# Performance work log

Hardware: AMD Instinct MI355X
Metric: run time of the kernel (lower is better)

## Reference

```python
import jax, jax.numpy as jnp
import numpy as np

B, L, DIM, H = 2, 2048, 2048, 16
D = DIM // H
EPS = 1e-6
CAP = 50.0
SCALE = D ** -0.5


def _rms_norm(x, w):
    # x: [B,H,L,D], normalize over last dim
    scale = jax.lax.rsqrt(jnp.maximum(jnp.mean(x * x, axis=-1, keepdims=True), EPS))
    return w * x * scale


def _rotate_half(x):
    x1, x2 = jnp.split(x, 2, axis=-1)
    return jnp.concatenate([-x2, x1], axis=-1)


def setup_inputs() -> dict:
    key = jax.random.key(0)
    ks = jax.random.split(key, 6)
    x = jax.random.normal(ks[0], (B, L, DIM), dtype=jnp.float32)
    w_qkv = jax.random.normal(ks[1], (3 * DIM, DIM), dtype=jnp.float32) * (DIM ** -0.5)
    w_out = jax.random.normal(ks[2], (DIM, DIM), dtype=jnp.float32) * (DIM ** -0.5)
    q_norm_w = jnp.ones((D,), dtype=jnp.float32)
    k_norm_w = jnp.ones((D,), dtype=jnp.float32)
    # rope tables [L, D]
    inv_freq = 1.0 / (10000.0 ** (np.arange(0, D, 2, dtype=np.float32) / D))
    t = np.arange(L, dtype=np.float32)
    freqs = np.outer(t, inv_freq)  # [L, D/2]
    emb = np.concatenate([freqs, freqs], axis=-1)  # [L, D]
    cos = jnp.asarray(np.cos(emb), dtype=jnp.float32)
    sin = jnp.asarray(np.sin(emb), dtype=jnp.float32)
    # additive causal mask [1,1,L,L]
    causal = np.triu(np.full((L, L), -1e9, dtype=np.float32), k=1)
    mask = jnp.asarray(causal)[None, None]
    return {"x": x, "w_qkv": w_qkv, "w_out": w_out, "q_norm_w": q_norm_w,
            "k_norm_w": k_norm_w, "cos": cos, "sin": sin, "mask": mask}


def reference(x, w_qkv, w_out, q_norm_w, k_norm_w, cos, sin, mask):
    b, l, _ = x.shape
    qkv = jnp.einsum('bld,ed->ble', x, w_qkv).reshape(b, l, 3, H, D)
    q, k, v = [jnp.transpose(qkv[:, :, i], (0, 2, 1, 3)) for i in range(3)]  # [B,H,L,D]
    q = _rms_norm(q, q_norm_w)
    k = _rms_norm(k, k_norm_w)
    # rope: cos/sin are [L,D] -> [1,1,L,D]
    c = cos[-l:, :][None, None]
    s = sin[-l:, :][None, None]
    q = q * c + _rotate_half(q) * s
    k = k * c + _rotate_half(k) * s
    attn = jnp.einsum('bhqd,bhkd->bhqk', q, k) * SCALE
    attn = jnp.tanh(attn / CAP) * CAP + mask
    probs = jax.nn.softmax(attn, axis=-1)
    o = jnp.einsum('bhqk,bhkd->bhqd', probs, v)
    o = jnp.transpose(o, (0, 2, 1, 3)).reshape(b, l, H * D)
    out = jnp.einsum('bld,ed->ble', o, w_out)
    return (out, (k, v))
```

## Files before the change

### kernel.cpp

```cpp
#include <hip/hip_runtime.h>
#include <hip/hip_bf16.h>
#include <stdint.h>

#define LL 2048
#define DD 128
#define HH 16

typedef float f32x4 __attribute__((ext_vector_type(4)));
typedef float f32x16 __attribute__((ext_vector_type(16)));
typedef float f32x2 __attribute__((ext_vector_type(2)));
typedef short bf16x8 __attribute__((ext_vector_type(8)));
typedef short short4v __attribute__((ext_vector_type(4)));
typedef int int4v __attribute__((ext_vector_type(4)));
typedef float float4v __attribute__((ext_vector_type(4)));

__device__ __forceinline__ float bf2f(short s) {
  union { unsigned u; float f; } v; v.u = ((unsigned)(unsigned short)s) << 16; return v.f;
}
__device__ __forceinline__ short f2bf(float f) {
  union { float f; unsigned u; } v; v.f = f;
  unsigned u = v.u;
  u += 0x7fffu + ((u >> 16) & 1u);
  return (short)(u >> 16);
}
__device__ __forceinline__ unsigned cvtpk(float lo, float hi) {
  unsigned r;
  asm("v_cvt_pk_bf16_f32 %0, %1, %2" : "=v"(r) : "v"(lo), "v"(hi));
  return r;
}

__device__ __forceinline__ void gload_lds16(const void* g, void* lds) {
  __builtin_amdgcn_global_load_lds(
      (__attribute__((address_space(1))) unsigned int*)(void*)(uintptr_t)g,
      (__attribute__((address_space(3))) unsigned int*)lds, 16, 0, 0);
}

__global__ __launch_bounds__(256) void cast_all_kernel(
    const float* __restrict__ x, const float* __restrict__ wqkv,
    const float* __restrict__ wout, short* __restrict__ dst)
{
  long i4 = ((long)blockIdx.x * 256 + threadIdx.x) * 4;
  const float* src; long off;
  if (i4 < 8388608L)        { src = x;    off = i4; }
  else if (i4 < 20971520L)  { src = wqkv; off = i4 - 8388608L; }
  else                      { src = wout; off = i4 - 20971520L; }
  float4v v = *(const float4v*)(src + off);
  short4v o;
  o.x = f2bf(v.x); o.y = f2bf(v.y); o.z = f2bf(v.z); o.w = f2bf(v.w);
  *(short4v*)(dst + i4) = o;
}

#define SCHED __builtin_amdgcn_sched_barrier(0)
#define BARRIER { __builtin_amdgcn_s_barrier(); }

#define STAGE(buf, opx, ptr, rb, ks, t)                                        \
  { _Pragma("unroll") for (int l_ = 0; l_ < 2; ++l_) {                          \
      int ch_ = l_ * 512 + tid;                                                 \
      int row_ = ch_ >> 2, ci_ = ch_ & 3;                                       \
      gload_lds16(ptr + (size_t)(rb + row_) * K + (t) * 64 + (ks) * 32 +        \
                      ((ci_ ^ ((row_ >> 1) & 3)) << 3),                         \
                  &lds[buf][opx][ks][ch_ << 3]);                                \
  } }

#define LDA(buf, mh, ks)                                                       \
  { _Pragma("unroll") for (int mf_ = 0; mf_ < 4; ++mf_) {                       \
      int r_ = wm * 128 + (mh) * 64 + mf_ * 16 + j;                             \
      areg[mf_] = *(const bf16x8*)&lds[buf][0][ks][r_ * 32 + ((g ^ ((j >> 1) & 3)) << 3)]; \
  } }

#define LDB(dst, buf, ks)                                                      \
  { _Pragma("unroll") for (int nf_ = 0; nf_ < 4; ++nf_) {                       \
      int r_ = wn * 64 + nf_ * 16 + j;                                          \
      dst[nf_] = *(const bf16x8*)&lds[buf][1][ks][r_ * 32 + ((g ^ ((j >> 1) & 3)) << 3)]; \
  } }

#define MFMAQ(mh, breg)                                                        \
  { __builtin_amdgcn_s_setprio(1);                                             \
    _Pragma("unroll") for (int mf_ = 0; mf_ < 4; ++mf_)                         \
      _Pragma("unroll") for (int nf_ = 0; nf_ < 4; ++nf_)                       \
        acc[(mh) * 4 + mf_][nf_] = __builtin_amdgcn_mfma_f32_16x16x32_bf16(     \
            areg[mf_], breg[nf_], acc[(mh) * 4 + mf_][nf_], 0, 0, 0);           \
    __builtin_amdgcn_s_setprio(0); }

__global__ __launch_bounds__(512, 2) void gemm256_kernel(
    const short* __restrict__ A, const short* __restrict__ Bm,
    short* __restrict__ C, int M, int N, int K)
{
  __shared__ __align__(16) short lds[2][2][2][8192];
  const int tid = threadIdx.x;
  const int lane = tid & 63;
  const int wid = tid >> 6;
  const int wm = wid >> 2, wn = wid & 3;
  const int g = lane >> 4, j = lane & 15;
  const int m0 = blockIdx.y * 256, n0 = blockIdx.x * 256;
  const int NT = K >> 6;

  f32x4 acc[8][4];
  const f32x4 z = {0.f, 0.f, 0.f, 0.f};
#pragma unroll
  for (int im = 0; im < 8; ++im)
#pragma unroll
    for (int nf = 0; nf < 4; ++nf) acc[im][nf] = z;

  STAGE(0, 1, Bm, n0, 0, 0); STAGE(0, 1, Bm, n0, 1, 0);
  STAGE(0, 0, A,  m0, 0, 0); STAGE(0, 0, A,  m0, 1, 0);
  STAGE(1, 1, Bm, n0, 0, 1); STAGE(1, 1, Bm, n0, 1, 1);
  STAGE(1, 0, A,  m0, 0, 1);
  asm volatile("s_waitcnt vmcnt(6)" ::: "memory");
  __builtin_amdgcn_s_barrier();
  SCHED;

  bf16x8 areg[4], b0r[4], b1r[4];
#pragma unroll 1
  for (int i = 0; i < (NT >> 1) - 1; ++i) {
    int t0 = i * 2;
    LDA(0, 0, 0); LDB(b0r, 0, 0);
    STAGE(1, 0, A, m0, 1, t0 + 1);
    BARRIER; MFMAQ(0, b0r); BARRIER;
    LDA(0, 0, 1); LDB(b1r, 0, 1);
    STAGE(0, 1, Bm, n0, 0, t0 + 2);
    BARRIER; MFMAQ(0, b1r); BARRIER;
    LDA(0, 1, 0);
    STAGE(0, 1, Bm, n0, 1, t0 + 2);
    BARRIER; MFMAQ(1, b0r); BARRIER;
    LDA(0, 1, 1);
    STAGE(0, 0, A, m0, 0, t0 + 2);
    BARRIER; MFMAQ(1, b1r);
    asm volatile("s_waitcnt vmcnt(6)" ::: "memory");
    __builtin_amdgcn_s_barrier(); SCHED;
    LDA(1, 0, 0); LDB(b0r, 1, 0);
    STAGE(0, 0, A, m0, 1, t0 + 2);
    BARRIER; MFMAQ(0, b0r); BARRIER;
    LDA(1, 0, 1); LDB(b1r, 1, 1);
    STAGE(1, 1, Bm, n0, 0, t0 + 3);
    BARRIER; MFMAQ(0, b1r); BARRIER;
    LDA(1, 1, 0);
    STAGE(1, 1, Bm, n0, 1, t0 + 3);
    BARRIER; MFMAQ(1, b0r); BARRIER;
    LDA(1, 1, 1);
    STAGE(1, 0, A, m0, 0, t0 + 3);
    BARRIER; MFMAQ(1, b1r);
    asm volatile("s_waitcnt vmcnt(6)" ::: "memory");
    __builtin_amdgcn_s_barrier(); SCHED;
  }
  {
    LDA(0, 0, 0); LDB(b0r, 0, 0);
    STAGE(1, 0, A, m0, 1, NT - 1);
    BARRIER; MFMAQ(0, b0r); BARRIER;
    LDA(0, 0, 1); LDB(b1r, 0, 1);
    BARRIER; MFMAQ(0, b1r); BARRIER;
    LDA(0, 1, 0);
    BARRIER; MFMAQ(1, b0r); BARRIER;
    LDA(0, 1, 1);
    BARRIER; MFMAQ(1, b1r);
    asm volatile("s_waitcnt vmcnt(0)" ::: "memory");
    __builtin_amdgcn_s_barrier(); SCHED;
    LDA(1, 0, 0); LDB(b0r, 1, 0); MFMAQ(0, b0r);
    LDA(1, 0, 1); LDB(b1r, 1, 1); MFMAQ(0, b1r);
    LDA(1, 1, 0); MFMAQ(1, b0r);
    LDA(1, 1, 1); MFMAQ(1, b1r);
  }
#pragma unroll
  for (int im = 0; im < 8; ++im)
#pragma unroll
    for (int nf = 0; nf < 4; ++nf)
#pragma unroll
      for (int r = 0; r < 4; ++r)
        C[(size_t)(m0 + wm * 128 + im * 16 + g * 4 + r) * N + n0 + wn * 64 + nf * 16 + j] =
            f2bf(acc[im][nf][r]);
}

template <typename OutT>
__global__ __launch_bounds__(256) void gemm_bt_kernel(
    const short* __restrict__ A, const short* __restrict__ Bm,
    OutT* __restrict__ C, int M, int N, int K)
{
  __shared__ __align__(16) short As[128 * 64];
  __shared__ __align__(16) short Bs[128 * 64];
  const int tid = threadIdx.x;
  const int lane = tid & 63;
  const int g = lane >> 4, j = lane & 15;
  const int m0 = blockIdx.y * 128, n0 = blockIdx.x * 128;
  const int wave = tid >> 6;
  const int wm = (wave >> 1) * 64, wn = (wave & 1) * 64;

  f32x4 acc[4][4];
  const f32x4 z = {0.f, 0.f, 0.f, 0.f};
#pragma unroll
  for (int i = 0; i < 4; ++i)
#pragma unroll
    for (int jj = 0; jj < 4; ++jj) acc[i][jj] = z;

  for (int k0 = 0; k0 < K; k0 += 64) {
#pragma unroll
    for (int it = 0; it < 4; ++it) {
      int c = it * 256 + tid;
      int row = c >> 3, ko = (c & 7) << 3;
      gload_lds16(A + (size_t)(m0 + row) * K + k0 + ko, As + c * 8);
    }
#pragma unroll
    for (int it = 0; it < 4; ++it) {
      int c = it * 256 + tid;
      int row = c >> 3, ko = (c & 7) << 3;
      gload_lds16(Bm + (size_t)(n0 + row) * K + k0 + ko, Bs + c * 8);
    }
    __syncthreads();
#pragma unroll
    for (int ks = 0; ks < 2; ++ks) {
      bf16x8 af[4], bfr[4];
#pragma unroll
      for (int i = 0; i < 4; ++i)
        af[i] = *(const bf16x8*)(As + (wm + i * 16 + j) * 64 + ks * 32 + g * 8);
#pragma unroll
      for (int i = 0; i < 4; ++i)
        bfr[i] = *(const bf16x8*)(Bs + (wn + i * 16 + j) * 64 + ks * 32 + g * 8);
#pragma unroll
      for (int i = 0; i < 4; ++i)
#pragma unroll
        for (int jj = 0; jj < 4; ++jj)
          acc[i][jj] = __builtin_amdgcn_mfma_f32_16x16x32_bf16(af[i], bfr[jj], acc[i][jj], 0, 0, 0);
    }
    __syncthreads();
  }
#pragma unroll
  for (int i = 0; i < 4; ++i)
#pragma unroll
    for (int jj = 0; jj < 4; ++jj)
#pragma unroll
      for (int r = 0; r < 4; ++r) {
        int row = m0 + wm + i * 16 + g * 4 + r;
        int col = n0 + wn + jj * 16 + j;
        if constexpr (sizeof(OutT) == 4)
          C[(size_t)row * N + col] = acc[i][jj][r];
        else
          C[(size_t)row * N + col] = f2bf(acc[i][jj][r]);
      }
}

__global__ __launch_bounds__(256) void normrope_kernel(
    const short* __restrict__ qkv, const float* __restrict__ qw,
    const float* __restrict__ kw, const float* __restrict__ cosb,
    const float* __restrict__ sinb, short* __restrict__ qo,
    float* __restrict__ ko, short* __restrict__ kb, float* __restrict__ vo)
{
  int wid = (blockIdx.x * 256 + threadIdx.x) >> 6;
  int lane = threadIdx.x & 63;
  int h = wid & 15;
  int rest = wid >> 4;
  int t = rest % 3;
  int bl = rest / 3;
  int l = bl & (LL - 1);
  int d0 = lane * 2;
  const short* src = qkv + (size_t)bl * 6144 + t * 2048 + h * 128 + d0;
  int raw = *(const int*)src;
  float v0 = bf2f((short)(raw & 0xffff));
  float v1 = bf2f((short)((raw >> 16) & 0xffff));
  size_t oidx = ((size_t)((bl >> 11) * HH + h) * LL + l) * DD + d0;
  if (t == 2) {
    f32x2 vv = {v0, v1};
    *(f32x2*)(vo + oidx) = vv;
    return;
  }
  float ss = v0 * v0 + v1 * v1;
#pragma unroll
  for (int m = 1; m <= 32; m <<= 1) ss += __shfl_xor(ss, m, 64);
  float scale = rsqrtf(fmaxf(ss * (1.0f / 128.0f), 1e-6f));
  const float* w = (t == 0) ? qw : kw;
  float n0 = w[d0] * v0 * scale;
  float n1 = w[d0 + 1] * v1 * scale;
  float c0 = cosb[l * 128 + d0], c1 = cosb[l * 128 + d0 + 1];
  float s0 = sinb[l * 128 + d0], s1 = sinb[l * 128 + d0 + 1];
  float p0 = __shfl_xor(n0, 32, 64);
  float p1 = __shfl_xor(n1, 32, 64);
  float r0 = (lane < 32) ? -p0 : p0;
  float r1 = (lane < 32) ? -p1 : p1;
  float o0 = n0 * c0 + r0 * s0;
  float o1 = n1 * c1 + r1 * s1;
  if (t == 0) {
    const float cu = 0.0017677669529663687f;
    int pk = (int)((unsigned short)f2bf(o0 * cu) |
                   ((unsigned)(unsigned short)f2bf(o1 * cu) << 16));
    *(int*)(qo + oidx) = pk;
  } else {
    f32x2 kk = {o0, o1};
    *(f32x2*)(ko + oidx) = kk;
    int pk = (int)((unsigned short)f2bf(o0) | ((unsigned)(unsigned short)f2bf(o1) << 16));
    *(int*)(kb + oidx) = pk;
  }
}

__global__ __launch_bounds__(256) void transpose_v_kernel(
    const short* __restrict__ qkv, short* __restrict__ vT)
{
  __shared__ __align__(16) short tl[64 * 72];
  int bid = blockIdx.x;
  int dt = bid & 1;
  int lt = (bid >> 1) & 31;
  int bh = bid >> 6;
  int b = bh >> 4, h = bh & 15;
  int tid = threadIdx.x;
#pragma unroll
  for (int it = 0; it < 2; ++it) {
    int c = it * 256 + tid;
    int row = c >> 3, off = (c & 7) << 3;
    int l = lt * 64 + row;
    bf16x8 val = *(const bf16x8*)(qkv + (size_t)(b * LL + l) * 6144 + 4096 + h * 128 + dt * 64 + off);
    *(bf16x8*)(tl + row * 72 + off) = val;
  }
  __syncthreads();
#pragma unroll
  for (int it = 0; it < 2; ++it) {
    int c = it * 256 + tid;
    int dr = c >> 3, lo = (c & 7) << 3;
    bf16x8 o;
#pragma unroll
    for (int i = 0; i < 8; ++i) o[i] = tl[(lo + i) * 72 + dr];
    *(bf16x8*)(vT + ((size_t)bh * DD + dt * 64 + dr) * LL + lt * 64 + lo) = o;
  }
}

__global__ __launch_bounds__(256, 2) void attn_kernel(
    const short* __restrict__ q, const short* __restrict__ k,
    const short* __restrict__ vT, short* __restrict__ o)
{
  __shared__ __align__(16) short Ks[64 * 128];
  __shared__ __align__(16) short Vs[128 * 64];
  int bid = blockIdx.x;
  int bh = bid & 31;
  int gq = (bid >> 5) & 7;
  int qt = (bid < 256) ? (15 - gq) : gq;
  int b = bh >> 4;
  int h = bh & 15;
  int tid = threadIdx.x;
  int lane = tid & 63;
  int w = tid >> 6;
  int l31 = lane & 31, lo5 = lane >> 5;
  int q0 = qt * 128;
  int wrow = q0 + w * 32;
  int qg = wrow + l31;

  const short* kp = k + (size_t)bh * LL * DD;
  const short* vp = vT + (size_t)bh * DD * LL;

  bf16x8 qf[8];
#pragma unroll
  for (int ds_ = 0; ds_ < 8; ++ds_)
    qf[ds_] = *(const bf16x8*)(q + ((size_t)bh * LL + qg) * DD + ds_ * 16 + lo5 * 8);

  f32x16 accO[4];
#pragma unroll
  for (int dt = 0; dt < 4; ++dt)
#pragma unroll
    for (int r = 0; r < 16; ++r) accO[dt][r] = 0.f;
  float lsum = 0.f;

  int ktmax = 2 * qt + 1;
  for (int kt = 0; kt <= ktmax; ++kt) {
    int k0 = kt * 64;
#pragma unroll
    for (int it = 0; it < 4; ++it) {
      int c = it * 256 + tid;
      int row = c >> 4, off = (c & 15) << 3;
      gload_lds16(kp + (size_t)(k0 + row) * DD + (off ^ ((row & 7) << 3)), Ks + c * 8);
    }
#pragma unroll
    for (int it = 0; it < 4; ++it) {
      int c = it * 256 + tid;
      int row = c >> 3, off = (c & 7) << 3;
      gload_lds16(vp + (size_t)row * LL + k0 + (off ^ ((row & 7) << 3)), Vs + c * 8);
    }
    __syncthreads();

    const bool active = (k0 <= wrow + 31);
    if (active) {
      f32x16 sa[2];
#pragma unroll
      for (int t2 = 0; t2 < 2; ++t2)
#pragma unroll
        for (int r = 0; r < 16; ++r) sa[t2][r] = 0.f;

      __builtin_amdgcn_s_setprio(1);
#pragma unroll
      for (int ds_ = 0; ds_ < 8; ++ds_) {
#pragma unroll
        for (int t2 = 0; t2 < 2; ++t2) {
          int row = t2 * 32 + l31;
          bf16x8 kf = *(const bf16x8*)(Ks + row * 128 +
                          ((ds_ * 16 + lo5 * 8) ^ ((l31 & 7) << 3)));
          sa[t2] = __builtin_amdgcn_mfma_f32_32x32x16_bf16(kf, qf[ds_], sa[t2], 0, 0, 0);
        }
      }
      __builtin_amdgcn_s_setprio(0);

#pragma unroll
      for (int t2 = 0; t2 < 2; ++t2) {
        const bool tmask = (k0 + t2 * 32 + 31) > wrow;
#pragma unroll
        for (int r = 0; r < 16; ++r) {
          float u = sa[t2][r];
          float v2 = u * u;
          float poly = fmaf(v2, fmaf(v2, fmaf(v2, -2.6984127f, 6.6666667f),
                                     -16.666667f), 50.f);
          float p = __expf(fmaf(u, poly, -12.f));
          int kglob = k0 + t2 * 32 + (r & 3) + 8 * (r >> 2) + 4 * lo5;
          if (tmask && (kglob > qg)) p = 0.f;
          lsum += p;
          sa[t2][r] = p;
        }
      }

      __builtin_amdgcn_s_setprio(1);
#pragma unroll
      for (int s = 0; s < 4; ++s) {
        int t2 = s >> 1, RA = 8 * (s & 1), RB = RA + 4;
        unsigned xa0 = cvtpk(sa[t2][RA + 0], sa[t2][RA + 1]);
        unsigned xa1 = cvtpk(sa[t2][RA + 2], sa[t2][RA + 3]);
        unsigned xb0 = cvtpk(sa[t2][RB + 0], sa[t2][RB + 1]);
        unsigned xb1 = cvtpk(sa[t2][RB + 2], sa[t2][RB + 3]);
        unsigned sxa0 = (unsigned)__shfl_xor((int)xa0, 32, 64);
        unsigned sxa1 = (unsigned)__shfl_xor((int)xa1, 32, 64);
        unsigned sxb0 = (unsigned)__shfl_xor((int)xb0, 32, 64);
        unsigned sxb1 = (unsigned)__shfl_xor((int)xb1, 32, 64);
        int4v wv;
        wv.x = (int)(lo5 ? sxb0 : xa0);
        wv.y = (int)(lo5 ? sxb1 : xa1);
        wv.z = (int)(lo5 ? xb0 : sxa0);
        wv.w = (int)(lo5 ? xb1 : sxa1);
        bf16x8 pa = __builtin_bit_cast(bf16x8, wv);
#pragma unroll
        for (int dt = 0; dt < 4; ++dt) {
          int row = dt * 32 + l31;
          bf16x8 vf = *(const bf16x8*)(Vs + row * 64 +
                          ((s * 16 + lo5 * 8) ^ ((l31 & 7) << 3)));
          accO[dt] = __builtin_amdgcn_mfma_f32_32x32x16_bf16(pa, vf, accO[dt], 0, 0, 0);
        }
      }
      __builtin_amdgcn_s_setprio(0);
    }
    __syncthreads();
  }

  lsum += __shfl_xor(lsum, 32, 64);
  float inv = 1.f / lsum;
#pragma unroll
  for (int r = 0; r < 16; ++r) {
    int qrow = (r & 3) + 8 * (r >> 2) + 4 * lo5;
    float invr = __shfl(inv, qrow, 64);
    size_t obase = ((size_t)b * LL + wrow + qrow) * 2048 + h * 128;
#pragma unroll
    for (int dt = 0; dt < 4; ++dt)
      o[obase + dt * 32 + l31] = f2bf(accO[dt][r] * invr);
  }
}

extern "C" void kernel_launch(void* const* d_in, const int* in_sizes, int n_in,
                              void* d_out, int out_size, void* d_ws, size_t ws_size,
                              hipStream_t stream) {
  const float* x    = (const float*)d_in[0];
  const float* wqkv = (const float*)d_in[1];
  const float* wout = (const float*)d_in[2];
  const float* qw   = (const float*)d_in[3];
  const float* kw   = (const float*)d_in[4];
  const float* cosb = (const float*)d_in[5];
  const float* sinb = (const float*)d_in[6];

  float* out   = (float*)d_out;
  float* k_out = out + 8388608;
  float* v_out = out + 16777216;

  short* ws    = (short*)d_ws;
  short* xb    = ws;
  short* wqkvb = ws + 8388608;
  short* woutb = ws + 20971520;
  short* qkv   = ws + 25165824;
  short* qbuf  = xb;
  short* kbuf  = wqkvb;
  short* vT    = ws + 50331648;
  short* obuf  = qkv;

  cast_all_kernel<<<24576, 256, 0, stream>>>(x, wqkv, wout, ws);
  gemm256_kernel<<<dim3(24, 16), 512, 0, stream>>>(xb, wqkvb, qkv, 4096, 6144, 2048);
  normrope_kernel<<<49152, 256, 0, stream>>>(qkv, qw, kw, cosb, sinb, qbuf, k_out, kbuf, v_out);
  transpose_v_kernel<<<2048, 256, 0, stream>>>(qkv, vT);
  attn_kernel<<<512, 256, 0, stream>>>(qbuf, kbuf, vT, obuf);
  gemm_bt_kernel<float><<<dim3(16, 32), 256, 0, stream>>>(obuf, woutb, out, 4096, 2048, 2048);
}
```

Measured before the change: 302.6 us.

## Double-buffer K/V tiles in attention kernel with async prefetch two tiles ahead

Gives the attention kernel two LDS buffers each for K and V. The tile for iteration kt+2 is issued while tile kt is being computed, with explicit vmcnt waits and barriers replacing the load-then-syncthreads pattern. The goal is to hide global-to-LDS load latency behind the MFMA and softmax work. LDS use doubles to 64KB per block, which may limit the two-blocks-per-CU occupancy.

After: 301.4 us. About the same (-0.4%).

```diff
diff --git a/kernel.cpp b/kernel.cpp
--- a/kernel.cpp
+++ b/kernel.cpp
@@ -319,12 +319,27 @@
   }
 }
 
+#define STAGE_KV(t, buf)                                                       \
+  { int k0_ = (t) * 64;                                                        \
+    _Pragma("unroll") for (int it_ = 0; it_ < 4; ++it_) {                      \
+      int c_ = it_ * 256 + tid;                                                \
+      int row_ = c_ >> 4, off_ = (c_ & 15) << 3;                               \
+      gload_lds16(kp + (size_t)(k0_ + row_) * DD + (off_ ^ ((row_ & 7) << 3)), \
+                  Ks[buf] + c_ * 8);                                           \
+    }                                                                          \
+    _Pragma("unroll") for (int it_ = 0; it_ < 4; ++it_) {                      \
+      int c_ = it_ * 256 + tid;                                                \
+      int row_ = c_ >> 3, off_ = (c_ & 7) << 3;                                \
+      gload_lds16(vp + (size_t)row_ * LL + k0_ + (off_ ^ ((row_ & 7) << 3)),   \
+                  Vs[buf] + c_ * 8);                                           \
+    } }
+
 __global__ __launch_bounds__(256, 2) void attn_kernel(
     const short* __restrict__ q, const short* __restrict__ k,
     const short* __restrict__ vT, short* __restrict__ o)
 {
-  __shared__ __align__(16) short Ks[64 * 128];
-  __shared__ __align__(16) short Vs[128 * 64];
+  __shared__ __align__(16) short Ks[2][64 * 128];
+  __shared__ __align__(16) short Vs[2][128 * 64];
   int bid = blockIdx.x;
   int bh = bid & 31;
   int gq = (bid >> 5) & 7;
@@ -355,21 +370,15 @@
   float lsum = 0.f;
 
   int ktmax = 2 * qt + 1;
+  STAGE_KV(0, 0);
+  STAGE_KV(1, 1);
+  asm volatile("s_waitcnt vmcnt(8)" ::: "memory");
+  __builtin_amdgcn_s_barrier();
+
   for (int kt = 0; kt <= ktmax; ++kt) {
     int k0 = kt * 64;
-#pragma unroll
-    for (int it = 0; it < 4; ++it) {
-      int c = it * 256 + tid;
-      int row = c >> 4, off = (c & 15) << 3;
-      gload_lds16(kp + (size_t)(k0 + row) * DD + (off ^ ((row & 7) << 3)), Ks + c * 8);
-    }
-#pragma unroll
-    for (int it = 0; it < 4; ++it) {
-      int c = it * 256 + tid;
-      int row = c >> 3, off = (c & 7) << 3;
-      gload_lds16(vp + (size_t)row * LL + k0 + (off ^ ((row & 7) << 3)), Vs + c * 8);
-    }
-    __syncthreads();
+    const short* Kb = Ks[kt & 1];
+    const short* Vb = Vs[kt & 1];
 
     const bool active = (k0 <= wrow + 31);
     if (active) {
@@ -385,7 +394,7 @@
 #pragma unroll
         for (int t2 = 0; t2 < 2; ++t2) {
           int row = t2 * 32 + l31;
-          bf16x8 kf = *(const bf16x8*)(Ks + row * 128 +
+          bf16x8 kf = *(const bf16x8*)(Kb + row * 128 +
                           ((ds_ * 16 + lo5 * 8) ^ ((l31 & 7) << 3)));
           sa[t2] = __builtin_amdgcn_mfma_f32_32x32x16_bf16(kf, qf[ds_], sa[t2], 0, 0, 0);
         }
@@ -430,14 +439,22 @@
 #pragma unroll
         for (int dt = 0; dt < 4; ++dt) {
           int row = dt * 32 + l31;
-          bf16x8 vf = *(const bf16x8*)(Vs + row * 64 +
+          bf16x8 vf = *(const bf16x8*)(Vb + row * 64 +
                           ((s * 16 + lo5 * 8) ^ ((l31 & 7) << 3)));
           accO[dt] = __builtin_amdgcn_mfma_f32_32x32x16_bf16(pa, vf, accO[dt], 0, 0, 0);
         }
       }
       __builtin_amdgcn_s_setprio(0);
     }
-    __syncthreads();
+
+    __builtin_amdgcn_s_barrier();
+    if (kt + 2 <= ktmax) {
+      STAGE_KV(kt + 2, kt & 1);
+      asm volatile("s_waitcnt vmcnt(8)" ::: "memory");
+    } else if (kt + 1 <= ktmax) {
+      asm volatile("s_waitcnt vmcnt(0)" ::: "memory");
+    }
+    __builtin_amdgcn_s_barrier();
   }
 
   lsum += __shfl_xor(lsum, 32, 64);
```
